# Kernel optimization log

Hardware: AMD Instinct MI355X
Metric: run time of the kernel (lower is better)

The kernel has to match this reference:

```python
import jax, jax.numpy as jnp
from jax import lax
import numpy as np

GAMMA = 0.1
INF = 1e9


def _softmin3(a, b, c, gamma):
    z = jnp.stack([a, b, c], axis=0)
    return -gamma * jax.nn.logsumexp(-z / gamma, axis=0)


def soft_dtw(x, y, gamma=GAMMA):
    """Batched soft-DTW with squared-Euclidean cost. x:[B,N,C], y:[B,M,C] -> [B]."""
    B, N, C = x.shape
    M = y.shape[1]
    # pairwise squared euclidean cost matrix D: [B, N, M]
    D = (jnp.sum(x * x, -1)[:, :, None]
         + jnp.sum(y * y, -1)[:, None, :]
         - 2.0 * jnp.einsum('bic,bjc->bij', x, y))
    ii = jnp.arange(N)

    def step(carry, p):
        r2, r1 = carry  # diagonals p-2 and p-1, each [B, N]; r1[i] = R[i, p-1-i]
        jj = p - ii
        valid = (jj >= 0) & (jj < M)
        jc = jnp.clip(jj, 0, M - 1)
        Dd = jnp.take_along_axis(D, jnp.broadcast_to(jc[None, :, None], (B, N, 1)), axis=2)[..., 0]
        corner = jnp.where(p == 0, 0.0, INF)  # R[-1,-1]=0 only reachable at p=0
        up = jnp.concatenate([jnp.full((B, 1), INF, D.dtype), r1[:, :-1]], axis=1)       # R[i-1, j]
        diag = jnp.concatenate([jnp.full((B, 1), 1.0, D.dtype) * corner, r2[:, :-1]], axis=1)  # R[i-1, j-1]
        left = r1                                                                          # R[i, j-1]
        r = Dd + _softmin3(up, left, diag, gamma)
        r = jnp.where(valid[None, :], r, INF)
        return (r1, r), None

    init = (jnp.full((B, N), INF, D.dtype), jnp.full((B, N), INF, D.dtype))
    (_, rlast), _ = lax.scan(step, init, jnp.arange(N + M - 1))
    return rlast[:, N - 1]  # R[N-1, M-1]


def setup_inputs() -> dict:
    key = jax.random.key(0)
    ks = jax.random.split(key, 7)
    B, S, T, C = 16, 128, 800, 80
    d = jax.random.uniform(ks[0], (B, S), jnp.float32) * 10.0
    mel_len = jax.random.randint(ks[1], (B,), 0, 800, jnp.int32)
    mel = jax.random.normal(ks[2], (B, T, C), jnp.float32)
    mel_postnet = jax.random.normal(ks[3], (B, T, C), jnp.float32)
    mel_target = jax.random.normal(ks[4], (B, T, C), jnp.float32)
    src_mask = jax.random.randint(ks[5], (B, S), 0, 2, jnp.int32).astype(bool)
    pred_mel_mask = jax.random.randint(ks[6], (B, T), 0, 2, jnp.int32).astype(bool)
    return {"d": d, "mel_len": mel_len, "mel": mel, "mel_postnet": mel_postnet,
            "mel_target": mel_target, "src_mask": src_mask, "pred_mel_mask": pred_mel_mask}


def reference(d, mel_len, mel, mel_postnet, mel_target, src_mask, pred_mel_mask):
    d = jnp.where(src_mask, 0.0, d)
    ones = jnp.where(src_mask, 0.0, 1.0)
    mel = jnp.where(pred_mel_mask[:, :, None], 0.0, mel)
    d_loss = jnp.mean(jnp.abs(mel_len.astype(d.dtype) - jnp.sum(d, axis=1)) / jnp.sum(ones, axis=1))
    mel_loss = 0.001 * jnp.mean(soft_dtw(jax.nn.sigmoid(mel), jax.nn.sigmoid(mel_target)))
    mel_postnet_loss = 0.001 * jnp.mean(soft_dtw(jax.nn.sigmoid(mel_postnet), jax.nn.sigmoid(mel_target)))
    return (mel_loss, mel_postnet_loss, d_loss)
```

## Files before the change

### kernel.cpp

```cpp
#include <hip/hip_runtime.h>
#include <hip/hip_fp16.h>

#define TT 800
#define CC 80
#define BB 16
#define SS 128
#define INFV 1e9f
#define NLCB 107
#define LAGCH 8
#define NGC 131
#define BANDH 200
#define HALF_PER_BAND (107*50*32)
#define HALF_PER_SLOT (4*107*50*32)
#define SCALE 14.426950408889634f
#define SIG_ELEMS (BB*TT*CC)
#define SIG_BYTES (3*SIG_ELEMS*2)
#define NROWS (3*BB*TT)
#define NORM_BYTES (NROWS*4)

typedef __attribute__((ext_vector_type(8))) _Float16 f16x8;
typedef __attribute__((ext_vector_type(4))) float f32x4;

__device__ inline bool mask_get(const void* p, int idx, int isInt) {
  if (isInt) return ((const int*)p)[idx] != 0;
  return ((const unsigned char*)p)[idx] != 0;
}

__device__ __forceinline__ float fexp2(float x) {
#if __has_builtin(__builtin_amdgcn_exp2f)
  return __builtin_amdgcn_exp2f(x);
#else
  return __expf(x * 0.6931471805599453f);
#endif
}
__device__ __forceinline__ float flog2(float x) {
#if __has_builtin(__builtin_amdgcn_logf)
  return __builtin_amdgcn_logf(x);
#else
  return __logf(x) * 1.4426950408889634f;
#endif
}
__device__ __forceinline__ float fmin3(float a, float b, float c) {
  return fminf(fminf(a, b), c);
}

__device__ __forceinline__ float shift_up1(float x) {
  int xi = __builtin_bit_cast(int, x);
  int b = __builtin_amdgcn_update_dpp(xi, xi, 0x143, 0xf, 0xf, false);
  b = __builtin_amdgcn_update_dpp(b, xi, 0x142, 0xf, 0xf, false);
  b = __builtin_amdgcn_update_dpp(b, xi, 0x111, 0xf, 0xf, false);
  return __builtin_bit_cast(float, b);
}

__global__ __launch_bounds__(256) void detect_dloss_kernel(
    const float* __restrict__ d, const int* __restrict__ mel_len,
    const void* __restrict__ src_mask, const void* __restrict__ pred_mask,
    int* __restrict__ flags, float* __restrict__ out)
{
  __shared__ int nzs, nzp;
  __shared__ float lb[BB];
  int tid = threadIdx.x;
  if (tid == 0) { nzs = 0; nzp = 0; }
  __syncthreads();
  const unsigned char* sm = (const unsigned char*)src_mask;
  const unsigned char* pm = (const unsigned char*)pred_mask;
  int f = 0;
  for (int i = tid; i < BB * SS; i += 256) if ((i & 3) && sm[i]) f = 1;
  if (f) atomicOr(&nzs, 1);
  f = 0;
  for (int i = tid; i < BB * TT; i += 256) if ((i & 3) && pm[i]) f = 1;
  if (f) atomicOr(&nzp, 1);
  __syncthreads();
  int isIntS = nzs ? 0 : 1;
  if (tid == 0) { flags[0] = isIntS; flags[1] = nzp ? 0 : 1; }

  int b = tid >> 4, k = tid & 15;
  float sd = 0.f, so = 0.f;
  for (int s = k; s < SS; s += 16) {
    bool m = mask_get(src_mask, b * SS + s, isIntS);
    if (!m) { sd += d[b * SS + s]; so += 1.f; }
  }
  for (int off = 8; off; off >>= 1) {
    sd += __shfl_down(sd, off, 16);
    so += __shfl_down(so, off, 16);
  }
  if (k == 0) lb[b] = fabsf((float)mel_len[b] - sd) / so;
  __syncthreads();
  if (tid == 0) {
    float s = 0.f;
    for (int i = 0; i < BB; i++) s += lb[i];
    out[2] = s / (float)BB;
  }
}

__global__ __launch_bounds__(256) void sig_kernel(
    const float* __restrict__ mel, const float* __restrict__ post,
    const float* __restrict__ target, const void* __restrict__ pred_mask,
    const int* __restrict__ flags, __half* __restrict__ sig)
{
  int arr = blockIdx.y;
  const float* src = arr == 0 ? mel : (arr == 1 ? post : target);
  __half* dst = sig + (size_t)arr * SIG_ELEMS;
  int pack = blockIdx.x * 256 + threadIdx.x;
  if (pack >= SIG_ELEMS / 8) return;
  size_t e0 = (size_t)pack * 8;
  float4 v0 = *(const float4*)(src + e0);
  float4 v1 = *(const float4*)(src + e0 + 4);
  if (arr == 0) {
    int bt = (int)(e0 / CC);
    if (mask_get(pred_mask, bt, flags[1])) {
      v0 = make_float4(0.f, 0.f, 0.f, 0.f);
      v1 = make_float4(0.f, 0.f, 0.f, 0.f);
    }
  }
  float f[8] = {v0.x, v0.y, v0.z, v0.w, v1.x, v1.y, v1.z, v1.w};
  union { __half h[8]; uint4 u; } o;
#pragma unroll
  for (int i = 0; i < 8; i++) o.h[i] = __float2half(1.f / (1.f + __expf(-f[i])));
  *(uint4*)(dst + e0) = o.u;
}

__global__ __launch_bounds__(256) void rnorm_kernel(
    const __half* __restrict__ sig, float* __restrict__ norms)
{
  int row = blockIdx.x * 256 + threadIdx.x;
  if (row >= NROWS) return;
  const __half* p = sig + (size_t)row * CC;
  float s = 0.f;
#pragma unroll
  for (int c = 0; c < CC; c += 8) {
    uint4 u = *(const uint4*)(p + c);
    const __half2* h2 = (const __half2*)&u;
#pragma unroll
    for (int q = 0; q < 4; q++) {
      float2 fv = __half22float2(h2[q]);
      s = fmaf(fv.x, fv.x, s);
      s = fmaf(fv.y, fv.y, s);
    }
  }
  norms[row] = s;
}

__global__ __launch_bounds__(64) void costm_kernel(
    const __half* __restrict__ sig, const float* __restrict__ norms,
    __half* __restrict__ Dsk, int probBase)
{
  int slot = blockIdx.y;
  int prob = probBase + slot;
  int which = prob >> 4, b = prob & 15;
  const __half* X = sig + (size_t)which * SIG_ELEMS + (size_t)b * TT * CC;
  const __half* Y = sig + (size_t)2 * SIG_ELEMS + (size_t)b * TT * CC;
  const float* nx = norms + which * (BB * TT) + b * TT;
  const float* ny = norms + 2 * (BB * TT) + b * TT;
  int lane = threadIdx.x;
  int mrow = lane & 15, kh = lane >> 4;
  int i0 = blockIdx.x * 16;

  const __half* xr = X + (size_t)(i0 + mrow) * CC;
  uint4 az0 = *(const uint4*)(xr + kh * 8);
  uint4 az1 = *(const uint4*)(xr + 32 + kh * 8);
  uint4 az2 = make_uint4(0, 0, 0, 0);
  if (kh < 2) az2 = *(const uint4*)(xr + 64 + kh * 8);
  f16x8 a0 = __builtin_bit_cast(f16x8, az0);
  f16x8 a1 = __builtin_bit_cast(f16x8, az1);
  f16x8 a2 = __builtin_bit_cast(f16x8, az2);

  int i4 = i0 + (lane >> 4) * 4;
  float4 nx4 = *(const float4*)(nx + i4);

  int band = i4 / BANDH;
  int l = (i4 % BANDH) >> 2;
  __half* obase = Dsk + (size_t)slot * HALF_PER_SLOT +
                  (size_t)band * HALF_PER_BAND + (size_t)l * 32;

  const __half* yr = Y + (size_t)mrow * CC;
  for (int j0 = 0; j0 < TT; j0 += 16) {
    uint4 bz0 = *(const uint4*)(yr + kh * 8);
    uint4 bz1 = *(const uint4*)(yr + 32 + kh * 8);
    uint4 bz2 = make_uint4(0, 0, 0, 0);
    if (kh < 2) bz2 = *(const uint4*)(yr + 64 + kh * 8);
    f32x4 acc = {0.f, 0.f, 0.f, 0.f};
    acc = __builtin_amdgcn_mfma_f32_16x16x32_f16(a0, __builtin_bit_cast(f16x8, bz0), acc, 0, 0, 0);
    acc = __builtin_amdgcn_mfma_f32_16x16x32_f16(a1, __builtin_bit_cast(f16x8, bz1), acc, 0, 0, 0);
    acc = __builtin_amdgcn_mfma_f32_16x16x32_f16(a2, __builtin_bit_cast(f16x8, bz2), acc, 0, 0, 0);

    int j = j0 + mrow;
    float nyv = ny[j];
    int s = j + l;
    int ch = s >> 3, kk = s & 7;
    union { __half h[4]; uint2 u; } cv;
#pragma unroll
    for (int r = 0; r < 4; r++) {
      float nxv = (r == 0) ? nx4.x : (r == 1) ? nx4.y : (r == 2) ? nx4.z : nx4.w;
      cv.h[r] = __float2half((nxv + nyv - 2.0f * acc[r]) * SCALE);
    }
    *(uint2*)(obase + (size_t)ch * 1600 + kk * 4) = cv.u;
    yr += (size_t)16 * CC;
  }
}

__global__ __launch_bounds__(256) void dtw_kernel(
    const __half* __restrict__ Dsk, float* __restrict__ out, int probBase)
{
  __shared__ float bnd[3][128];
  const int tid = threadIdx.x;
  const int w = tid >> 6, lane = tid & 63;
  const int slot = blockIdx.x;
  const int prob = probBase + slot;
  const int which = prob >> 4;
  const int lclamp = lane < 49 ? lane : 49;
  const __half* Db = Dsk + (size_t)slot * HALF_PER_SLOT + (size_t)w * HALF_PER_BAND;

  float cur0 = INFV, cur1 = INFV, cur2 = INFV, cur3 = INFV;
  float up_pipe = INFV, rcarry = INFV, res = 0.f;
  float rbv[8], wrv[8];
#pragma unroll
  for (int k = 0; k < 8; k++) { rbv[k] = INFV; wrv[k] = INFV; }

  uint4 a0, a1, a2, a3, b0, b1, b2, b3;

#define PRE(P0, P1, P2, P3, LCN) do { if ((LCN) < NLCB) {                     \
    const uint4* p_ = (const uint4*)(Db + ((size_t)(LCN) * 50 + lclamp) * 32);\
    P0 = p_[0]; P1 = p_[1]; P2 = p_[2]; P3 = p_[3]; } } while (0)

#define RINGLOAD do { if (w) {                                                \
    const float4* rp_ = (const float4*)&bnd[w - 1][s0 & 127];                 \
    float4 ra_ = rp_[0], rc_ = rp_[1];                                        \
    rbv[0] = ra_.x; rbv[1] = ra_.y; rbv[2] = ra_.z; rbv[3] = ra_.w;           \
    rbv[4] = rc_.x; rbv[5] = rc_.y; rbv[6] = rc_.z; rbv[7] = rc_.w; } } while (0)

#define DO_STEP(K, LOU, HIU) do {                                             \
    const int s_ = s0 + (K);                                                  \
    float nxt_ = shift_up1(cur3);      \
    unsigned lou_ = (LOU), hiu_ = (HIU);                                      \
    float2 f01 = __half22float2(*(const __half2*)&lou_);                      \
    float2 f23 = __half22float2(*(const __half2*)&hiu_);                      \
    float up_ = nxt_, dg_ = up_pipe;    \
    if (w == 0) { if (lane == 0) { up_ = INFV; dg_ = (s_ == 0) ? 0.0f : INFV; } } \
    else if (lane == 0) { up_ = rbv[(K)]; dg_ = ((K) == 0) ? rcarry : rbv[(K) == 0 ? 0 : (K) - 1]; } \
    float oc0 = cur0, oc1 = cur1, oc2 = cur2;                                 \
    float A0 = fmin3(up_, cur0, dg_);                                         \
    float m0 = f01.x + A0;                                                    \
    float sv0 = fexp2(A0 - up_) + fexp2(A0 - cur0) + fexp2(A0 - dg_);         \
    float A1 = fmin3(m0, cur1, oc0);                                          \
    float m1 = f01.y + A1;                                                    \
    float sv1 = fmaf(sv0, fexp2(A1 - m0), fexp2(A1 - cur1) + fexp2(A1 - oc0));\
    float A2 = fmin3(m1, cur2, oc1);                                          \
    float m2 = f23.x + A2;                                                    \
    float sv2 = fmaf(sv1, fexp2(A2 - m1), fexp2(A2 - cur2) + fexp2(A2 - oc1));\
    float A3 = fmin3(m2, cur3, oc2);                                          \
    float m3 = f23.y + A3;                                                    \
    float sv3 = fmaf(sv2, fexp2(A3 - m2), fexp2(A3 - cur3) + fexp2(A3 - oc2));\
    float r0 = m0 - flog2(sv0);                                               \
    float r1 = m1 - flog2(sv1);                                               \
    float r2 = m2 - flog2(sv2);                                               \
    float r3 = m3 - flog2(sv3);                                               \
    int j_ = s_ - lane;                                                       \
    bool act_ = (lane < 50) && ((unsigned)j_ < 800u);                         \
    cur0 = act_ ? r0 : INFV; cur1 = act_ ? r1 : INFV;                         \
    cur2 = act_ ? r2 : INFV; cur3 = act_ ? r3 : INFV;                         \
    wrv[(K)] = cur3;                                                          \
    if (s_ == 848) res = cur3;                                                \
    up_pipe = nxt_;                                                           \
  } while (0)

#define STEP8(Q0, Q1, Q2, Q3) do {                                            \
    DO_STEP(0, Q0.x, Q0.y); DO_STEP(1, Q0.z, Q0.w);                           \
    DO_STEP(2, Q1.x, Q1.y); DO_STEP(3, Q1.z, Q1.w);                           \
    DO_STEP(4, Q2.x, Q2.y); DO_STEP(5, Q2.z, Q2.w);                           \
    DO_STEP(6, Q3.x, Q3.y); DO_STEP(7, Q3.z, Q3.w); } while (0)

  PRE(a0, a1, a2, a3, 0);
  __syncthreads();

  for (int G = 0; G < NGC; ++G) {
    const int lc = G - LAGCH * w;
    if (lc >= 0 && lc < NLCB) {
      const int s0 = lc << 3;
      if ((lc & 1) == 0) {
        PRE(b0, b1, b2, b3, lc + 1);
        RINGLOAD;
        STEP8(a0, a1, a2, a3);
      } else {
        PRE(a0, a1, a2, a3, lc + 1);
        RINGLOAD;
        STEP8(b0, b1, b2, b3);
      }
      if (w < 3 && lane == 49) {
#pragma unroll
        for (int k = 0; k < 8; k++) {
          int j = s0 + k - 49;
          if ((unsigned)j < 800u) bnd[w][j & 127] = wrv[k];
        }
      }
      rcarry = rbv[7];
    }
    __syncthreads();
  }

  if (w == 3 && lane == 49) atomicAdd(&out[which], res * 4.3321699e-6f);

#undef PRE
#undef RINGLOAD
#undef DO_STEP
#undef STEP8
}

extern "C" void kernel_launch(void* const* d_in, const int* in_sizes, int n_in,
                              void* d_out, int out_size, void* d_ws, size_t ws_size,
                              hipStream_t stream) {
  const float* d         = (const float*)d_in[0];
  const int*   mel_len   = (const int*)d_in[1];
  const float* mel       = (const float*)d_in[2];
  const float* post      = (const float*)d_in[3];
  const float* target    = (const float*)d_in[4];
  const void*  src_mask  = d_in[5];
  const void*  pred_mask = d_in[6];
  float* out = (float*)d_out;

  int* flags = (int*)d_ws;
  __half* sig = (__half*)((char*)d_ws + 256);
  float* norms = (float*)((char*)d_ws + 256 + SIG_BYTES);
  __half* Dsk = (__half*)((char*)d_ws + 256 + SIG_BYTES + NORM_BYTES);
  size_t per = (size_t)HALF_PER_SLOT * sizeof(__half);
  size_t hdr = 256 + (size_t)SIG_BYTES + (size_t)NORM_BYTES;
  int slots = 0;
  if (ws_size > hdr) slots = (int)((ws_size - hdr) / per);
  if (slots > 32) slots = 32;

  (void)hipMemsetAsync(d_out, 0, 3 * sizeof(float), stream);
  detect_dloss_kernel<<<1, 256, 0, stream>>>(d, mel_len, src_mask, pred_mask, flags, out);
  if (slots < 1) return;
  sig_kernel<<<dim3(500, 3), 256, 0, stream>>>(mel, post, target, pred_mask, flags, sig);
  rnorm_kernel<<<150, 256, 0, stream>>>(sig, norms);

  for (int base = 0; base < 32; base += slots) {
    int g = (32 - base < slots) ? (32 - base) : slots;
    costm_kernel<<<dim3(50, g), 64, 0, stream>>>(sig, norms, Dsk, base);
    dtw_kernel<<<g, 256, 0, stream>>>(Dsk, out, base);
  }
}
```

Baseline: 288.6 us.

## Split DTW wavefront into two 400-row bands with 8 rows per lane

Each DTW block now uses two wavefronts instead of four. Every lane handles 8 consecutive rows instead of 4, so each band covers 400 rows, and the cost-matrix layout is reshaped to match. This cuts the pipeline fill and drain lag from three band hand-offs to one, reducing the total number of chunk steps. In exchange, each step carries a longer serial dependency chain per lane and needs more registers for double-buffered loads, which may lengthen per-step latency.

```diff
diff --git a/kernel.cpp b/kernel.cpp
--- a/kernel.cpp
+++ b/kernel.cpp
@@ -8,10 +8,10 @@
 #define INFV 1e9f
 #define NLCB 107
 #define LAGCH 8
-#define NGC 131
-#define BANDH 200
-#define HALF_PER_BAND (107*50*32)
-#define HALF_PER_SLOT (4*107*50*32)
+#define NGC 115
+#define BANDH 400
+#define HALF_PER_BAND (107*50*64)
+#define HALF_PER_SLOT (2*107*50*64)
 #define SCALE 14.426950408889634f
 #define SIG_ELEMS (BB*TT*CC)
 #define SIG_BYTES (3*SIG_ELEMS*2)
@@ -169,9 +169,10 @@
   float4 nx4 = *(const float4*)(nx + i4);
 
   int band = i4 / BANDH;
-  int l = (i4 % BANDH) >> 2;
+  int l = (i4 % BANDH) >> 3;
+  int rr4 = i4 & 7;
   __half* obase = Dsk + (size_t)slot * HALF_PER_SLOT +
-                  (size_t)band * HALF_PER_BAND + (size_t)l * 32;
+                  (size_t)band * HALF_PER_BAND + (size_t)l * 64 + rr4;
 
   const __half* yr = Y + (size_t)mrow * CC;
   for (int j0 = 0; j0 < TT; j0 += 16) {
@@ -194,15 +195,15 @@
       float nxv = (r == 0) ? nx4.x : (r == 1) ? nx4.y : (r == 2) ? nx4.z : nx4.w;
       cv.h[r] = __float2half((nxv + nyv - 2.0f * acc[r]) * SCALE);
     }
-    *(uint2*)(obase + (size_t)ch * 1600 + kk * 4) = cv.u;
+    *(uint2*)(obase + (size_t)ch * 3200 + kk * 8) = cv.u;
     yr += (size_t)16 * CC;
   }
 }
 
-__global__ __launch_bounds__(256) void dtw_kernel(
+__global__ __launch_bounds__(128) void dtw_kernel(
     const __half* __restrict__ Dsk, float* __restrict__ out, int probBase)
 {
-  __shared__ float bnd[3][128];
+  __shared__ float bnd[1][128];
   const int tid = threadIdx.x;
   const int w = tid >> 6, lane = tid & 63;
   const int slot = blockIdx.x;
@@ -211,66 +212,85 @@
   const int lclamp = lane < 49 ? lane : 49;
   const __half* Db = Dsk + (size_t)slot * HALF_PER_SLOT + (size_t)w * HALF_PER_BAND;
 
-  float cur0 = INFV, cur1 = INFV, cur2 = INFV, cur3 = INFV;
+  float c0 = INFV, c1 = INFV, c2 = INFV, c3 = INFV;
+  float c4 = INFV, c5 = INFV, c6 = INFV, c7 = INFV;
   float up_pipe = INFV, rcarry = INFV, res = 0.f;
   float rbv[8], wrv[8];
 #pragma unroll
   for (int k = 0; k < 8; k++) { rbv[k] = INFV; wrv[k] = INFV; }
 
-  uint4 a0, a1, a2, a3, b0, b1, b2, b3;
-
-#define PRE(P0, P1, P2, P3, LCN) do { if ((LCN) < NLCB) {                     \
-    const uint4* p_ = (const uint4*)(Db + ((size_t)(LCN) * 50 + lclamp) * 32);\
-    P0 = p_[0]; P1 = p_[1]; P2 = p_[2]; P3 = p_[3]; } } while (0)
+  uint4 a0, a1, a2, a3, a4, a5, a6, a7;
+  uint4 b0, b1, b2, b3, b4, b5, b6, b7;
+
+#define PRE(P0, P1, P2, P3, P4, P5, P6, P7, LCN) do { if ((LCN) < NLCB) {     \
+    const uint4* p_ = (const uint4*)(Db + ((size_t)(LCN) * 50 + lclamp) * 64);\
+    P0 = p_[0]; P1 = p_[1]; P2 = p_[2]; P3 = p_[3];                           \
+    P4 = p_[4]; P5 = p_[5]; P6 = p_[6]; P7 = p_[7]; } } while (0)
 
 #define RINGLOAD do { if (w) {                                                \
-    const float4* rp_ = (const float4*)&bnd[w - 1][s0 & 127];                 \
+    const float4* rp_ = (const float4*)&bnd[0][s0 & 127];                     \
     float4 ra_ = rp_[0], rc_ = rp_[1];                                        \
     rbv[0] = ra_.x; rbv[1] = ra_.y; rbv[2] = ra_.z; rbv[3] = ra_.w;           \
     rbv[4] = rc_.x; rbv[5] = rc_.y; rbv[6] = rc_.z; rbv[7] = rc_.w; } } while (0)
 
-#define DO_STEP(K, LOU, HIU) do {                                             \
+#define DO_STEP(K, Q) do {                                                    \
     const int s_ = s0 + (K);                                                  \
-    float nxt_ = shift_up1(cur3);      \
-    unsigned lou_ = (LOU), hiu_ = (HIU);                                      \
-    float2 f01 = __half22float2(*(const __half2*)&lou_);                      \
-    float2 f23 = __half22float2(*(const __half2*)&hiu_);                      \
-    float up_ = nxt_, dg_ = up_pipe;    \
+    float nxt_ = shift_up1(c7);        \
+    float2 f01 = __half22float2(*(const __half2*)&Q.x);                       \
+    float2 f23 = __half22float2(*(const __half2*)&Q.y);                       \
+    float2 f45 = __half22float2(*(const __half2*)&Q.z);                       \
+    float2 f67 = __half22float2(*(const __half2*)&Q.w);                       \
+    float up_ = nxt_, dg_ = up_pipe;            \
     if (w == 0) { if (lane == 0) { up_ = INFV; dg_ = (s_ == 0) ? 0.0f : INFV; } } \
     else if (lane == 0) { up_ = rbv[(K)]; dg_ = ((K) == 0) ? rcarry : rbv[(K) == 0 ? 0 : (K) - 1]; } \
-    float oc0 = cur0, oc1 = cur1, oc2 = cur2;                                 \
-    float A0 = fmin3(up_, cur0, dg_);                                         \
+    float A0 = fmin3(up_, c0, dg_);                                           \
     float m0 = f01.x + A0;                                                    \
-    float sv0 = fexp2(A0 - up_) + fexp2(A0 - cur0) + fexp2(A0 - dg_);         \
-    float A1 = fmin3(m0, cur1, oc0);                                          \
+    float s0v = fexp2(A0 - up_) + fexp2(A0 - c0) + fexp2(A0 - dg_);           \
+    float A1 = fmin3(m0, c1, c0);                                             \
     float m1 = f01.y + A1;                                                    \
-    float sv1 = fmaf(sv0, fexp2(A1 - m0), fexp2(A1 - cur1) + fexp2(A1 - oc0));\
-    float A2 = fmin3(m1, cur2, oc1);                                          \
+    float s1v = fmaf(s0v, fexp2(A1 - m0), fexp2(A1 - c1) + fexp2(A1 - c0));   \
+    float A2 = fmin3(m1, c2, c1);                                             \
     float m2 = f23.x + A2;                                                    \
-    float sv2 = fmaf(sv1, fexp2(A2 - m1), fexp2(A2 - cur2) + fexp2(A2 - oc1));\
-    float A3 = fmin3(m2, cur3, oc2);                                          \
+    float s2v = fmaf(s1v, fexp2(A2 - m1), fexp2(A2 - c2) + fexp2(A2 - c1));   \
+    float A3 = fmin3(m2, c3, c2);                                             \
     float m3 = f23.y + A3;                                                    \
-    float sv3 = fmaf(sv2, fexp2(A3 - m2), fexp2(A3 - cur3) + fexp2(A3 - oc2));\
-    float r0 = m0 - flog2(sv0);                                               \
-    float r1 = m1 - flog2(sv1);                                               \
-    float r2 = m2 - flog2(sv2);                                               \
-    float r3 = m3 - flog2(sv3);                                               \
+    float s3v = fmaf(s2v, fexp2(A3 - m2), fexp2(A3 - c3) + fexp2(A3 - c2));   \
+    float A4 = fmin3(m3, c4, c3);                                             \
+    float m4 = f45.x + A4;                                                    \
+    float s4v = fmaf(s3v, fexp2(A4 - m3), fexp2(A4 - c4) + fexp2(A4 - c3));   \
+    float A5 = fmin3(m4, c5, c4);                                             \
+    float m5 = f45.y + A5;                                                    \
+    float s5v = fmaf(s4v, fexp2(A5 - m4), fexp2(A5 - c5) + fexp2(A5 - c4));   \
+    float A6 = fmin3(m5, c6, c5);                                             \
+    float m6 = f67.x + A6;                                                    \
+    float s6v = fmaf(s5v, fexp2(A6 - m5), fexp2(A6 - c6) + fexp2(A6 - c5));   \
+    float A7 = fmin3(m6, c7, c6);                                             \
+    float m7 = f67.y + A7;                                                    \
+    float s7v = fmaf(s6v, fexp2(A7 - m6), fexp2(A7 - c7) + fexp2(A7 - c6));   \
+    float r0 = m0 - flog2(s0v);                                               \
+    float r1 = m1 - flog2(s1v);                                               \
+    float r2 = m2 - flog2(s2v);                                               \
+    float r3 = m3 - flog2(s3v);                                               \
+    float r4 = m4 - flog2(s4v);                                               \
+    float r5 = m5 - flog2(s5v);                                               \
+    float r6 = m6 - flog2(s6v);                                               \
+    float r7 = m7 - flog2(s7v);                                               \
     int j_ = s_ - lane;                                                       \
     bool act_ = (lane < 50) && ((unsigned)j_ < 800u);                         \
-    cur0 = act_ ? r0 : INFV; cur1 = act_ ? r1 : INFV;                         \
-    cur2 = act_ ? r2 : INFV; cur3 = act_ ? r3 : INFV;                         \
-    wrv[(K)] = cur3;                                                          \
-    if (s_ == 848) res = cur3;                                                \
+    c0 = act_ ? r0 : INFV; c1 = act_ ? r1 : INFV;                             \
+    c2 = act_ ? r2 : INFV; c3 = act_ ? r3 : INFV;                             \
+    c4 = act_ ? r4 : INFV; c5 = act_ ? r5 : INFV;                             \
+    c6 = act_ ? r6 : INFV; c7 = act_ ? r7 : INFV;                             \
+    wrv[(K)] = c7;                                                            \
+    if (s_ == 848) res = c7;                                                  \
     up_pipe = nxt_;                                                           \
   } while (0)
 
-#define STEP8(Q0, Q1, Q2, Q3) do {                                            \
-    DO_STEP(0, Q0.x, Q0.y); DO_STEP(1, Q0.z, Q0.w);                           \
-    DO_STEP(2, Q1.x, Q1.y); DO_STEP(3, Q1.z, Q1.w);                           \
-    DO_STEP(4, Q2.x, Q2.y); DO_STEP(5, Q2.z, Q2.w);                           \
-    DO_STEP(6, Q3.x, Q3.y); DO_STEP(7, Q3.z, Q3.w); } while (0)
-
-  PRE(a0, a1, a2, a3, 0);
+#define STEP8(Q0, Q1, Q2, Q3, Q4, Q5, Q6, Q7) do {                            \
+    DO_STEP(0, Q0); DO_STEP(1, Q1); DO_STEP(2, Q2); DO_STEP(3, Q3);           \
+    DO_STEP(4, Q4); DO_STEP(5, Q5); DO_STEP(6, Q6); DO_STEP(7, Q7); } while (0)
+
+  PRE(a0, a1, a2, a3, a4, a5, a6, a7, 0);
   __syncthreads();
 
   for (int G = 0; G < NGC; ++G) {
@@ -278,19 +298,19 @@
     if (lc >= 0 && lc < NLCB) {
       const int s0 = lc << 3;
       if ((lc & 1) == 0) {
-        PRE(b0, b1, b2, b3, lc + 1);
+        PRE(b0, b1, b2, b3, b4, b5, b6, b7, lc + 1);
         RINGLOAD;
-        STEP8(a0, a1, a2, a3);
+        STEP8(a0, a1, a2, a3, a4, a5, a6, a7);
       } else {
-        PRE(a0, a1, a2, a3, lc + 1);
+        PRE(a0, a1, a2, a3, a4, a5, a6, a7, lc + 1);
         RINGLOAD;
-        STEP8(b0, b1, b2, b3);
+        STEP8(b0, b1, b2, b3, b4, b5, b6, b7);
       }
-      if (w < 3 && lane == 49) {
+      if (w == 0 && lane == 49) {
 #pragma unroll
         for (int k = 0; k < 8; k++) {
           int j = s0 + k - 49;
-          if ((unsigned)j < 800u) bnd[w][j & 127] = wrv[k];
+          if ((unsigned)j < 800u) bnd[0][j & 127] = wrv[k];
         }
       }
       rcarry = rbv[7];
@@ -298,7 +318,7 @@
     __syncthreads();
   }
 
-  if (w == 3 && lane == 49) atomicAdd(&out[which], res * 4.3321699e-6f);
+  if (w == 1 && lane == 49) atomicAdd(&out[which], res * 4.3321699e-6f);
 
 #undef PRE
 #undef RINGLOAD
@@ -337,6 +357,6 @@
   for (int base = 0; base < 32; base += slots) {
     int g = (32 - base < slots) ? (32 - base) : slots;
     costm_kernel<<<dim3(50, g), 64, 0, stream>>>(sig, norms, Dsk, base);
-    dtw_kernel<<<g, 256, 0, stream>>>(Dsk, out, base);
-  }
-}
+    dtw_kernel<<<g, 128, 0, stream>>>(Dsk, out, base);
+  }
+}
```

After: 373.6 us. 29.4% more time.
